# Kernel tuning notes

Measured on AMD Instinct MI355X. Metric: run time of the kernel, lower is better.

The kernel has to match this reference:

```python
import jax, jax.numpy as jnp
import numpy as np

B, S, H = 2, 2048, 1024
NH = 16
HD = H // NH

def setup_inputs() -> dict:
    key = jax.random.key(0)
    ks = jax.random.split(key, 9)
    s = 1.0 / np.sqrt(H)
    return {
        "hidden_state": jax.random.normal(ks[0], (B, S, H), dtype=jnp.float32),
        "Wq": jax.random.normal(ks[1], (H, H), dtype=jnp.float32) * s,
        "bq": jnp.zeros((H,), dtype=jnp.float32),
        "Wk": jax.random.normal(ks[2], (H, H), dtype=jnp.float32) * s,
        "bk": jnp.zeros((H,), dtype=jnp.float32),
        "Wv": jax.random.normal(ks[3], (H, H), dtype=jnp.float32) * s,
        "bv": jnp.zeros((H,), dtype=jnp.float32),
        "Wo": jax.random.normal(ks[4], (H, H), dtype=jnp.float32) * s,
        "bo": jnp.zeros((H,), dtype=jnp.float32),
    }

def reference(hidden_state, Wq, bq, Wk, bk, Wv, bv, Wo, bo):
    x = hidden_state  # [B,S,H]
    def split(t):
        return t.reshape(B, S, NH, HD).transpose(0, 2, 1, 3)  # [B,NH,S,HD]
    q = split(x @ Wq.T + bq)
    k = split(x @ Wk.T + bk)
    v = split(x @ Wv.T + bv)
    scale = 1.0 / jnp.sqrt(jnp.asarray(HD, dtype=x.dtype))
    scores = jnp.einsum('bhqd,bhkd->bhqk', q, k) * scale  # [B,NH,S,S]
    probs = jax.nn.softmax(scores, axis=-1)
    out = jnp.einsum('bhqk,bhkd->bhqd', probs, v)  # [B,NH,S,HD]
    out = out.transpose(0, 2, 1, 3).reshape(B, S, H)
    return out @ Wo.T + bo
```

## Files before the change

kernel.cpp:

```cpp
#include <hip/hip_runtime.h>


#define BD 2
#define SD 2048
#define HDIM 1024
#define NHD 16
#define HDD 64
#define NTOK 4096
#define QSCALE 0.1803368801111204f

typedef float f32x4 __attribute__((ext_vector_type(4)));
typedef _Float16 f16x8 __attribute__((ext_vector_type(8)));
typedef _Float16 f16x4 __attribute__((ext_vector_type(4)));
typedef __fp16 fp16x2 __attribute__((ext_vector_type(2)));

__device__ __forceinline__ f32x4 mfma_f16(f16x8 a, f16x8 b, f32x4 c) {
  return __builtin_amdgcn_mfma_f32_16x16x32_f16(a, b, c, 0, 0, 0);
}

__device__ __forceinline__ unsigned int pk2h(float lo, float hi) {
  fp16x2 v = __builtin_amdgcn_cvt_pkrtz(lo, hi);
  return __builtin_bit_cast(unsigned int, v);
}

__global__ void convert_kernel(const float* __restrict__ x,
                               const float* __restrict__ wq, const float* __restrict__ wk,
                               const float* __restrict__ wv, const float* __restrict__ wo,
                               _Float16* __restrict__ dst) {
  const int total4 = (8 * 1024 * 1024) / 4;
  for (int idx = blockIdx.x * blockDim.x + threadIdx.x; idx < total4;
       idx += gridDim.x * blockDim.x) {
    int e = idx * 4;
    const float* s;
    if (e < 4 * 1024 * 1024) {
      s = x + e;
    } else {
      int w = (e - 4 * 1024 * 1024) >> 20;
      int off = e & 1048575;
      s = (w == 0 ? wq : w == 1 ? wk : w == 2 ? wv : wo) + off;
    }
    float4 v = *(const float4*)s;
    f16x4 h;
    h[0] = (_Float16)v.x; h[1] = (_Float16)v.y;
    h[2] = (_Float16)v.z; h[3] = (_Float16)v.w;
    *(f16x4*)(dst + e) = h;
  }
}

__device__ __forceinline__ void gemm_mainloop(
    const _Float16* __restrict__ Ap, const _Float16* __restrict__ Bp,
    int i0, int j0, _Float16* As, _Float16* Bs, f32x4 acc[4][4]) {
  const int tid = threadIdx.x;
  const int wid = tid >> 6, lane = tid & 63;
  const int lr = lane & 15, lg = lane >> 4;
  const int wm = wid >> 1, wn = wid & 1;
  const int srow = lane >> 2;
  const int scol = (lane & 3) * 8;

  for (int k0 = 0; k0 < HDIM; k0 += 32) {
#pragma unroll
    for (int it = 0; it < 2; ++it) {
      int rb = (wid * 2 + it) * 16;
      const _Float16* ga = Ap + (size_t)(i0 + rb + srow) * HDIM + k0 + scol;
      const _Float16* gb = Bp + (size_t)(j0 + rb + srow) * HDIM + k0 + scol;
      __builtin_amdgcn_global_load_lds(
          (__attribute__((address_space(1))) void*)ga,
          (__attribute__((address_space(3))) void*)(As + (wid * 2 + it) * 512), 16, 0, 0);
      __builtin_amdgcn_global_load_lds(
          (__attribute__((address_space(1))) void*)gb,
          (__attribute__((address_space(3))) void*)(Bs + (wid * 2 + it) * 512), 16, 0, 0);
    }
    __syncthreads();
    f16x8 af[4], bf[4];
#pragma unroll
    for (int mt = 0; mt < 4; mt++)
      af[mt] = *(const f16x8*)(As + (wm * 64 + mt * 16 + lr) * 32 + lg * 8);
#pragma unroll
    for (int nt = 0; nt < 4; nt++)
      bf[nt] = *(const f16x8*)(Bs + (wn * 64 + nt * 16 + lr) * 32 + lg * 8);
#pragma unroll
    for (int mt = 0; mt < 4; mt++)
#pragma unroll
      for (int nt = 0; nt < 4; nt++)
        acc[mt][nt] = mfma_f16(af[mt], bf[nt], acc[mt][nt]);
    __syncthreads();
  }
}

__global__ __launch_bounds__(256) void gemm_qkv(
    const _Float16* __restrict__ xb,
    const _Float16* __restrict__ wqb, const _Float16* __restrict__ wkb,
    const _Float16* __restrict__ wvb,
    const float* __restrict__ bq, const float* __restrict__ bk,
    const float* __restrict__ bv,
    _Float16* __restrict__ Qo, _Float16* __restrict__ Ko, _Float16* __restrict__ Vt) {
  __shared__ __attribute__((aligned(16))) _Float16 As[128 * 32];
  __shared__ __attribute__((aligned(16))) _Float16 Bs[128 * 32];
  const int bx = blockIdx.x;
  const int mat = bx >> 8;
  const int sub = bx & 255;
  const _Float16 *Ap, *Bp;
  int i0, j0;
  if (mat < 2) {
    Ap = xb; Bp = (mat ? wkb : wqb);
    i0 = (sub >> 3) * 128;
    j0 = (sub & 7) * 128;
  } else {
    Ap = wvb; Bp = xb;
    i0 = (sub & 7) * 128;
    j0 = (sub >> 3) * 128;
  }
  f32x4 acc[4][4];
#pragma unroll
  for (int a = 0; a < 4; a++)
#pragma unroll
    for (int b = 0; b < 4; b++) acc[a][b] = (f32x4){0.f, 0.f, 0.f, 0.f};

  gemm_mainloop(Ap, Bp, i0, j0, As, Bs, acc);

  const int tid = threadIdx.x;
  const int wid = tid >> 6, lane = tid & 63;
  const int lr = lane & 15, lg = lane >> 4;
  const int wm = wid >> 1, wn = wid & 1;
  const float* bias = (mat == 0 ? bq : mat == 1 ? bk : bv);

#pragma unroll
  for (int mt = 0; mt < 4; mt++) {
#pragma unroll
    for (int nt = 0; nt < 4; nt++) {
      int i = i0 + wm * 64 + mt * 16 + 4 * lg;
      int j = j0 + wn * 64 + nt * 16 + lr;
      if (mat < 2) {
        float bj = bias[j];
        int h = j >> 6, d = j & 63;
        _Float16* dst = (mat ? Ko : Qo);
        float scl = (mat == 0) ? QSCALE : 1.0f;
#pragma unroll
        for (int r = 0; r < 4; r++) {
          int tok = i + r;
          int b = tok >> 11, s = tok & 2047;
          dst[(((size_t)(b * NHD + h)) * SD + s) * HDD + d] =
              (_Float16)((acc[mt][nt][r] + bj) * scl);
        }
      } else {
        int tok = j;
        int b = tok >> 11, s = tok & 2047;
#pragma unroll
        for (int r = 0; r < 4; r++) {
          int wr = i + r;
          int h = wr >> 6, d = wr & 63;
          Vt[((size_t)(b * NHD + h) * HDD + d) * SD + s] =
              (_Float16)(acc[mt][nt][r] + bias[wr]);
        }
      }
    }
  }
}

__global__ __launch_bounds__(256) void gemm_out(
    const _Float16* __restrict__ attn, const _Float16* __restrict__ wob,
    const float* __restrict__ bo, float* __restrict__ out) {
  __shared__ __attribute__((aligned(16))) _Float16 As[128 * 32];
  __shared__ __attribute__((aligned(16))) _Float16 Bs[128 * 32];
  const int sub = blockIdx.x;
  const int i0 = (sub >> 3) * 128, j0 = (sub & 7) * 128;
  f32x4 acc[4][4];
#pragma unroll
  for (int a = 0; a < 4; a++)
#pragma unroll
    for (int b = 0; b < 4; b++) acc[a][b] = (f32x4){0.f, 0.f, 0.f, 0.f};

  gemm_mainloop(attn, wob, i0, j0, As, Bs, acc);

  const int tid = threadIdx.x;
  const int wid = tid >> 6, lane = tid & 63;
  const int lr = lane & 15, lg = lane >> 4;
  const int wm = wid >> 1, wn = wid & 1;
#pragma unroll
  for (int mt = 0; mt < 4; mt++) {
#pragma unroll
    for (int nt = 0; nt < 4; nt++) {
      int i = i0 + wm * 64 + mt * 16 + 4 * lg;
      int j = j0 + wn * 64 + nt * 16 + lr;
      float bj = bo[j];
#pragma unroll
      for (int r = 0; r < 4; r++)
        out[(size_t)(i + r) * HDIM + j] = acc[mt][nt][r] + bj;
    }
  }
}

__global__ __launch_bounds__(512) void attn_kernel(
    const _Float16* __restrict__ Q, const _Float16* __restrict__ K,
    const _Float16* __restrict__ VT, _Float16* __restrict__ AO) {
  const int bh = blockIdx.y, qb = blockIdx.x;
  const int tid = threadIdx.x, wv = tid >> 6, lane = tid & 63;
  const int lr = lane & 15, lg = lane >> 4;
  const int q0 = qb * 128 + wv * 16;
  const _Float16* Qh = Q + (size_t)bh * SD * HDD;
  const _Float16* Kh = K + (size_t)bh * SD * HDD;
  const _Float16* Vh = VT + (size_t)bh * HDD * SD;

  __shared__ __attribute__((aligned(16))) _Float16 Ks[2][2][64][32];
  __shared__ __attribute__((aligned(16))) _Float16 Vs[2][2][64][32];

  const int krow = lane >> 2;
  const int kswz = (((lane & 3) ^ ((lane >> 3) & 3)) * 8);
  const int kkf = wv & 1, krb = (wv >> 1) * 16;

  const int m  = lane & 15;
  const int u  = m & 3;
  const int sg = m >> 2;
  const int r4 = lane >> 4;
  const int c2 = (r4 >> 1) & 1;
  const int keyoff_e = 16 * (u >> 1) + 4 * (sg ^ c2)       + 2 * (u & 1);
  const int keyoff_o = 16 * (u >> 1) + 4 * (sg ^ (c2 | 2)) + 2 * (u & 1);
  const _Float16* Vrow[2];
  Vrow[0] = Vh + (size_t)(wv * 8 + 0 + r4) * SD + keyoff_e;
  Vrow[1] = Vh + (size_t)(wv * 8 + 4 + r4) * SD + keyoff_o;

  auto stage = [&](int b, int kv0) {
    const _Float16* gk = Kh + (size_t)(kv0 + krb + krow) * HDD + kkf * 32 + kswz;
    __builtin_amdgcn_global_load_lds(
        (__attribute__((address_space(1))) void*)gk,
        (__attribute__((address_space(3))) void*)(&Ks[b][kkf][krb][0]), 16, 0, 0);
#pragma unroll
    for (int kf = 0; kf < 2; kf++)
#pragma unroll
      for (int i = 0; i < 2; i++) {
        const _Float16* gv = Vrow[i] + kv0 + kf * 32;
        __builtin_amdgcn_global_load_lds(
            (__attribute__((address_space(1))) void*)gv,
            (__attribute__((address_space(3))) void*)(&Vs[b][kf][wv * 8 + i * 4][0]), 4, 0, 0);
      }
  };

  const int fswz = (lg ^ ((lr >> 1) & 3)) * 8;

  f16x8 qf[2];
#pragma unroll
  for (int kf = 0; kf < 2; kf++)
    qf[kf] = *(const f16x8*)(Qh + (size_t)(q0 + lr) * HDD + kf * 32 + lg * 8);

  f32x4 acc[4];
#pragma unroll
  for (int i = 0; i < 4; i++) acc[i] = (f32x4){0.f, 0.f, 0.f, 0.f};
  float mrun = -1e30f, lsum = 0.f;

  stage(0, 0);
  int cur = 0;

  for (int t = 0; t < SD / 64; ++t) {
    asm volatile("s_waitcnt vmcnt(0)" ::: "memory");
    __builtin_amdgcn_s_barrier();
    stage(cur ^ 1, ((t + 1) & (SD / 64 - 1)) * 64);

    f32x4 sc[4];
#pragma unroll
    for (int nt = 0; nt < 4; nt++) sc[nt] = (f32x4){0.f, 0.f, 0.f, 0.f};
#pragma unroll
    for (int nt = 0; nt < 4; nt++)
#pragma unroll
      for (int kf = 0; kf < 2; kf++) {
        f16x8 kfr = *(const f16x8*)&Ks[cur][kf][nt * 16 + lr][fswz];
        sc[nt] = mfma_f16(kfr, qf[kf], sc[nt]);
      }

    float tm = sc[0][0];
#pragma unroll
    for (int nt = 0; nt < 4; nt++)
#pragma unroll
      for (int r = 0; r < 4; r++) tm = fmaxf(tm, sc[nt][r]);
    tm = fmaxf(tm, __shfl_xor(tm, 16));
    tm = fmaxf(tm, __shfl_xor(tm, 32));

    if (__any(tm - mrun > 8.0f)) {
      float mn = fmaxf(mrun, tm);
      float fm = exp2f(mrun - mn);
      mrun = mn;
      lsum *= fm;
#pragma unroll
      for (int ntd = 0; ntd < 4; ntd++)
#pragma unroll
        for (int r = 0; r < 4; r++) acc[ntd][r] *= fm;
    }

    float p[4][4];
#pragma unroll
    for (int nt = 0; nt < 4; nt++)
#pragma unroll
      for (int r = 0; r < 4; r++) {
        p[nt][r] = exp2f(sc[nt][r] - mrun);
        lsum += p[nt][r];
      }

#pragma unroll
    for (int kf = 0; kf < 2; kf++) {
      unsigned int pw[4];
      pw[0] = pk2h(p[2 * kf][0], p[2 * kf][1]);
      pw[1] = pk2h(p[2 * kf][2], p[2 * kf][3]);
      pw[2] = pk2h(p[2 * kf + 1][0], p[2 * kf + 1][1]);
      pw[3] = pk2h(p[2 * kf + 1][2], p[2 * kf + 1][3]);
      f16x8 pb = __builtin_bit_cast(f16x8, *(unsigned int(*)[4])pw);
#pragma unroll
      for (int ntd = 0; ntd < 4; ntd++) {
        f16x8 vf = *(const f16x8*)&Vs[cur][kf][ntd * 16 + lr][fswz];
        acc[ntd] = mfma_f16(vf, pb, acc[ntd]);
      }
    }
    cur ^= 1;
  }

  lsum += __shfl_xor(lsum, 16);
  lsum += __shfl_xor(lsum, 32);
  float inv = 1.0f / lsum;

  const int b = bh >> 4, h = bh & 15;
  _Float16* aoRow = AO + (size_t)(b * SD + q0 + lr) * HDIM + h * 64;
#pragma unroll
  for (int ntd = 0; ntd < 4; ntd++) {
    f16x4 o;
#pragma unroll
    for (int r = 0; r < 4; r++) o[r] = (_Float16)(acc[ntd][r] * inv);
    *(f16x4*)(aoRow + ntd * 16 + 4 * lg) = o;
  }
}

extern "C" void kernel_launch(void* const* d_in, const int* in_sizes, int n_in,
                              void* d_out, int out_size, void* d_ws, size_t ws_size,
                              hipStream_t stream) {
  const float* x  = (const float*)d_in[0];
  const float* Wq = (const float*)d_in[1];
  const float* bq = (const float*)d_in[2];
  const float* Wk = (const float*)d_in[3];
  const float* bk = (const float*)d_in[4];
  const float* Wv = (const float*)d_in[5];
  const float* bv = (const float*)d_in[6];
  const float* Wo = (const float*)d_in[7];
  const float* bo = (const float*)d_in[8];
  float* out = (float*)d_out;

  _Float16* xb  = (_Float16*)d_ws;
  _Float16* wqb = xb + 4 * 1024 * 1024;
  _Float16* wkb = wqb + 1024 * 1024;
  _Float16* wvb = wkb + 1024 * 1024;
  _Float16* wob = wvb + 1024 * 1024;
  _Float16* Qb  = wob + 1024 * 1024;
  _Float16* Kb  = Qb + 4 * 1024 * 1024;
  _Float16* Vt  = Kb + 4 * 1024 * 1024;
  _Float16* AOb = Vt + 4 * 1024 * 1024;

  convert_kernel<<<dim3(1024), dim3(256), 0, stream>>>(x, Wq, Wk, Wv, Wo, xb);
  gemm_qkv<<<dim3(768), dim3(256), 0, stream>>>(xb, wqb, wkb, wvb, bq, bk, bv, Qb, Kb, Vt);
  attn_kernel<<<dim3(16, 32), dim3(512), 0, stream>>>(Qb, Kb, Vt, AOb);
  gemm_out<<<dim3(256), dim3(256), 0, stream>>>(AOb, wob, bo, out);
}
```

Measured before the change: 140.5 us.

## Remap attention blocks per XCD, add MFMA priority hints, and split softmax ILP

Switches the attention grid to 1D and remaps block ids so every (batch, head) pair's query blocks land on the same XCD, which should improve L2 reuse of K/V. Wraps the MFMA sections in s_setprio raises so matrix work from one wave can overlap softmax math from others. Splits the max reduction into a tree and the row sum into four partial accumulators to shorten dependency chains. It also interleaves exp and PV MFMA per half-tile. This adds code complexity and slightly changes summation order.

```diff
diff --git a/kernel.cpp b/kernel.cpp
--- a/kernel.cpp
+++ b/kernel.cpp
@@ -193,7 +193,10 @@
 __global__ __launch_bounds__(512) void attn_kernel(
     const _Float16* __restrict__ Q, const _Float16* __restrict__ K,
     const _Float16* __restrict__ VT, _Float16* __restrict__ AO) {
-  const int bh = blockIdx.y, qb = blockIdx.x;
+  const int g = blockIdx.x;
+  const int xcd = g & 7, idx = g >> 3;
+  const int qb = idx & 15;
+  const int bh = xcd * 4 + (idx >> 4);
   const int tid = threadIdx.x, wv = tid >> 6, lane = tid & 63;
   const int lr = lane & 15, lg = lane >> 4;
   const int q0 = qb * 128 + wv * 16;
@@ -245,7 +248,8 @@
   f32x4 acc[4];
 #pragma unroll
   for (int i = 0; i < 4; i++) acc[i] = (f32x4){0.f, 0.f, 0.f, 0.f};
-  float mrun = -1e30f, lsum = 0.f;
+  float mrun = -1e30f;
+  float ls0 = 0.f, ls1 = 0.f, ls2 = 0.f, ls3 = 0.f;
 
   stage(0, 0);
   int cur = 0;
@@ -258,6 +262,7 @@
     f32x4 sc[4];
 #pragma unroll
     for (int nt = 0; nt < 4; nt++) sc[nt] = (f32x4){0.f, 0.f, 0.f, 0.f};
+    __builtin_amdgcn_s_setprio(1);
 #pragma unroll
     for (int nt = 0; nt < 4; nt++)
 #pragma unroll
@@ -265,12 +270,14 @@
         f16x8 kfr = *(const f16x8*)&Ks[cur][kf][nt * 16 + lr][fswz];
         sc[nt] = mfma_f16(kfr, qf[kf], sc[nt]);
       }
-
-    float tm = sc[0][0];
-#pragma unroll
-    for (int nt = 0; nt < 4; nt++)
-#pragma unroll
-      for (int r = 0; r < 4; r++) tm = fmaxf(tm, sc[nt][r]);
+    __builtin_amdgcn_s_setprio(0);
+
+    float t0 = fmaxf(fmaxf(sc[0][0], sc[0][1]), sc[0][2]);
+    float t1 = fmaxf(fmaxf(sc[0][3], sc[1][0]), sc[1][1]);
+    float t2 = fmaxf(fmaxf(sc[1][2], sc[1][3]), sc[2][0]);
+    float t3 = fmaxf(fmaxf(sc[2][1], sc[2][2]), sc[2][3]);
+    float t4 = fmaxf(fmaxf(sc[3][0], sc[3][1]), sc[3][2]);
+    float tm = fmaxf(fmaxf(fmaxf(t0, t1), fmaxf(t2, t3)), fmaxf(t4, sc[3][3]));
     tm = fmaxf(tm, __shfl_xor(tm, 16));
     tm = fmaxf(tm, __shfl_xor(tm, 32));
 
@@ -278,39 +285,57 @@
       float mn = fmaxf(mrun, tm);
       float fm = exp2f(mrun - mn);
       mrun = mn;
-      lsum *= fm;
+      ls0 *= fm; ls1 *= fm; ls2 *= fm; ls3 *= fm;
 #pragma unroll
       for (int ntd = 0; ntd < 4; ntd++)
 #pragma unroll
         for (int r = 0; r < 4; r++) acc[ntd][r] *= fm;
     }
 
-    float p[4][4];
-#pragma unroll
-    for (int nt = 0; nt < 4; nt++)
-#pragma unroll
-      for (int r = 0; r < 4; r++) {
-        p[nt][r] = exp2f(sc[nt][r] - mrun);
-        lsum += p[nt][r];
-      }
-
-#pragma unroll
-    for (int kf = 0; kf < 2; kf++) {
+    {
+      float p0[4], p1[4];
+#pragma unroll
+      for (int r = 0; r < 4; r++) p0[r] = exp2f(sc[0][r] - mrun);
+#pragma unroll
+      for (int r = 0; r < 4; r++) p1[r] = exp2f(sc[1][r] - mrun);
+      ls0 += (p0[0] + p0[1]) + (p0[2] + p0[3]);
+      ls1 += (p1[0] + p1[1]) + (p1[2] + p1[3]);
       unsigned int pw[4];
-      pw[0] = pk2h(p[2 * kf][0], p[2 * kf][1]);
-      pw[1] = pk2h(p[2 * kf][2], p[2 * kf][3]);
-      pw[2] = pk2h(p[2 * kf + 1][0], p[2 * kf + 1][1]);
-      pw[3] = pk2h(p[2 * kf + 1][2], p[2 * kf + 1][3]);
+      pw[0] = pk2h(p0[0], p0[1]); pw[1] = pk2h(p0[2], p0[3]);
+      pw[2] = pk2h(p1[0], p1[1]); pw[3] = pk2h(p1[2], p1[3]);
       f16x8 pb = __builtin_bit_cast(f16x8, *(unsigned int(*)[4])pw);
+      __builtin_amdgcn_s_setprio(1);
 #pragma unroll
       for (int ntd = 0; ntd < 4; ntd++) {
-        f16x8 vf = *(const f16x8*)&Vs[cur][kf][ntd * 16 + lr][fswz];
+        f16x8 vf = *(const f16x8*)&Vs[cur][0][ntd * 16 + lr][fswz];
         acc[ntd] = mfma_f16(vf, pb, acc[ntd]);
       }
+      __builtin_amdgcn_s_setprio(0);
+    }
+    {
+      float p0[4], p1[4];
+#pragma unroll
+      for (int r = 0; r < 4; r++) p0[r] = exp2f(sc[2][r] - mrun);
+#pragma unroll
+      for (int r = 0; r < 4; r++) p1[r] = exp2f(sc[3][r] - mrun);
+      ls2 += (p0[0] + p0[1]) + (p0[2] + p0[3]);
+      ls3 += (p1[0] + p1[1]) + (p1[2] + p1[3]);
+      unsigned int pw[4];
+      pw[0] = pk2h(p0[0], p0[1]); pw[1] = pk2h(p0[2], p0[3]);
+      pw[2] = pk2h(p1[0], p1[1]); pw[3] = pk2h(p1[2], p1[3]);
+      f16x8 pb = __builtin_bit_cast(f16x8, *(unsigned int(*)[4])pw);
+      __builtin_amdgcn_s_setprio(1);
+#pragma unroll
+      for (int ntd = 0; ntd < 4; ntd++) {
+        f16x8 vf = *(const f16x8*)&Vs[cur][1][ntd * 16 + lr][fswz];
+        acc[ntd] = mfma_f16(vf, pb, acc[ntd]);
+      }
+      __builtin_amdgcn_s_setprio(0);
     }
     cur ^= 1;
   }
 
+  float lsum = (ls0 + ls1) + (ls2 + ls3);
   lsum += __shfl_xor(lsum, 16);
   lsum += __shfl_xor(lsum, 32);
   float inv = 1.0f / lsum;
@@ -352,6 +377,6 @@
 
   convert_kernel<<<dim3(1024), dim3(256), 0, stream>>>(x, Wq, Wk, Wv, Wo, xb);
   gemm_qkv<<<dim3(768), dim3(256), 0, stream>>>(xb, wqb, wkb, wvb, bq, bk, bv, Qb, Kb, Vt);
-  attn_kernel<<<dim3(16, 32), dim3(512), 0, stream>>>(Qb, Kb, Vt, AOb);
+  attn_kernel<<<dim3(512), dim3(512), 0, stream>>>(Qb, Kb, Vt, AOb);
   gemm_out<<<dim3(256), dim3(256), 0, stream>>>(AOb, wob, bo, out);
 }
```

New measurement: 139.4 us. No clear change (-0.8%).
